# Performance work log

Hardware: AMD Instinct MI355X
Metric: run time of the kernel (lower is better)

Reference implementation:

```python
import jax, jax.numpy as jnp
import numpy as np

K = 20          # number of NAG iterations (init kwarg k)
MU = 0.05       # strong-convexity constant mu (init kwarg, fixed so no eigendecomp)
B, N = 4096, 128


def setup_inputs() -> dict:
    key = jax.random.key(0)
    k1, k2 = jax.random.split(key)
    w = jax.random.normal(k1, (B, N, N), dtype=jnp.float32)
    b = jax.random.normal(k2, (B, N), dtype=jnp.float32)
    s = jnp.asarray(1e-3, dtype=jnp.float32)  # learned step-size Parameter
    return {"w": w, "b": b, "s": s}


def reference(w, b, s):
    # NAG.forward with mu fixed, x_init=y_init=None (zeros), return_all=False.
    mu = jnp.asarray(MU, dtype=s.dtype)
    sqms = jnp.sqrt(mu * s)
    alpha = (1.0 - sqms) / (1.0 + sqms)  # scalar momentum coefficient

    x0 = jnp.zeros_like(b)
    y0 = jnp.zeros_like(b)

    def step(carry, _):
        x, y = carry
        # GD.gradient_decent(s, y, w, b): x_next = y - s * (w @ y - b)
        grad = jnp.einsum('bij,bj->bi', w, y) - b
        x_next = y - s * grad
        y_new = (1.0 + alpha) * x_next - alpha * x
        return (x_next, y_new), None

    (x, y), _ = jax.lax.scan(step, (x0, y0), None, length=K)
    return (x, y)
```

## Files before the change

### kernel.cpp

```cpp
#include <hip/hip_runtime.h>

#define K_ITERS 20
#define MU_CONST 0.05f
#define BN 128
#define YSTRIDE 24

typedef float v4f __attribute__((ext_vector_type(4)));
typedef __attribute__((address_space(1))) const v4f gc4;
typedef __attribute__((address_space(1))) v4f g4;

template <int CTRL>
__device__ __forceinline__ float dpp_add(float v) {
    int x = __builtin_amdgcn_update_dpp(0, __float_as_int(v), CTRL, 0xF, 0xF, true);
    return v + __int_as_float(x);
}
__device__ __forceinline__ float reduce8(float v) {
    v = dpp_add<0xB1>(v);
    v = dpp_add<0x4E>(v);
    v = dpp_add<0x141>(v);
    return v;
}

__global__ __launch_bounds__(256, 4) void nag_kernel(
    const float* __restrict__ w,
    const float* __restrict__ bvec,
    const float* __restrict__ s_ptr,
    float* __restrict__ out,
    int B)
{
    __shared__ __align__(16) float y_lds[2][8 * YSTRIDE];

    const int t  = threadIdx.x;
    const int wv = t >> 6;
    const int q  = (t >> 3) & 7;
    const int g  = t & 7;
    const int row0   = wv * 32 + q * 4;
    const int wslice = (row0 >> 4) * YSTRIDE + (q & 3) * 4;
    const int rbase  = g * YSTRIDE;

    const int batch = blockIdx.x;

    v4f w4[4][4];
    const gc4* wp = (const gc4*)(w + (size_t)batch * (BN * BN)
                                   + (size_t)row0 * BN + g * 16);
#pragma unroll
    for (int rho = 0; rho < 4; ++rho)
#pragma unroll
        for (int k = 0; k < 4; ++k)
            w4[rho][k] = wp[rho * 32 + k];

    const v4f br4 = *(const gc4*)(bvec + (size_t)batch * BN + row0);
    const float br_[4] = {br4.x, br4.y, br4.z, br4.w};

    const float s     = *s_ptr;
    const float sqms  = sqrtf(MU_CONST * s);
    const float alpha = (1.0f - sqms) / (1.0f + sqms);
    const float ap1   = 1.0f + alpha;

    float xs[4], ys[4];
#pragma unroll
    for (int rho = 0; rho < 4; ++rho) {
        xs[rho] = s * br_[rho];
        ys[rho] = ap1 * xs[rho];
    }
    if (g == 0)
        *reinterpret_cast<v4f*>(&y_lds[0][wslice]) =
            (v4f){ys[0], ys[1], ys[2], ys[3]};
    __syncthreads();

#pragma unroll 2
    for (int it = 1; it < K_ITERS; ++it) {
        const float* yb = &y_lds[(it + 1) & 1][rbase];
        v4f yv[4];
#pragma unroll
        for (int k = 0; k < 4; ++k)
            yv[k] = *reinterpret_cast<const v4f*>(yb + k * 4);

#pragma unroll
        for (int rho = 0; rho < 4; ++rho) {
            float p = w4[rho][0].x * yv[0].x;
            p = fmaf(w4[rho][0].y, yv[0].y, p);
            p = fmaf(w4[rho][0].z, yv[0].z, p);
            p = fmaf(w4[rho][0].w, yv[0].w, p);
            p = fmaf(w4[rho][1].x, yv[1].x, p);
            p = fmaf(w4[rho][1].y, yv[1].y, p);
            p = fmaf(w4[rho][1].z, yv[1].z, p);
            p = fmaf(w4[rho][1].w, yv[1].w, p);
            p = fmaf(w4[rho][2].x, yv[2].x, p);
            p = fmaf(w4[rho][2].y, yv[2].y, p);
            p = fmaf(w4[rho][2].z, yv[2].z, p);
            p = fmaf(w4[rho][2].w, yv[2].w, p);
            p = fmaf(w4[rho][3].x, yv[3].x, p);
            p = fmaf(w4[rho][3].y, yv[3].y, p);
            p = fmaf(w4[rho][3].z, yv[3].z, p);
            p = fmaf(w4[rho][3].w, yv[3].w, p);
            const float d  = reduce8(p);
            const float xn = fmaf(-s, d - br_[rho], ys[rho]);
            ys[rho] = fmaf(ap1, xn, -(alpha * xs[rho]));
            xs[rho] = xn;
        }

        if (it != K_ITERS - 1 && g == 0)
            *reinterpret_cast<v4f*>(&y_lds[it & 1][wslice]) =
                (v4f){ys[0], ys[1], ys[2], ys[3]};
        __syncthreads();
    }

    const size_t ob = (size_t)batch * BN + row0;
    if (g == 0)
        *(g4*)(out + ob) = (v4f){xs[0], xs[1], xs[2], xs[3]};
    else if (g == 1)
        *(g4*)(out + (size_t)B * BN + ob) = (v4f){ys[0], ys[1], ys[2], ys[3]};
}

extern "C" void kernel_launch(void* const* d_in, const int* in_sizes, int n_in,
                              void* d_out, int out_size, void* d_ws, size_t ws_size,
                              hipStream_t stream) {
    const float* w = (const float*)d_in[0];
    const float* b = (const float*)d_in[1];
    const float* s = (const float*)d_in[2];
    float* out = (float*)d_out;
    const int B = in_sizes[1] / BN;
    nag_kernel<<<dim3(B), dim3(256), 0, stream>>>(w, b, s, out, B);
}
```

Measured before the change: 60.67 us.

## Stage W loads through LDS with double-buffered direct global-to-LDS copies

Each wave now pulls its 32-row slice of W into a per-wave, double-buffered LDS staging area using global_load_lds, four sub-chunks at a time. Explicit vmcnt and lgkmcnt waits keep two chunks in flight while threads copy their rows from LDS into registers. The aim is fully coalesced, contiguous global reads and overlap of load latency with the register fill. In exchange it adds 32KB of LDS per block, which may limit occupancy, plus an extra LDS round trip on a kernel that is largely bandwidth bound.

```diff
diff --git a/kernel.cpp b/kernel.cpp
--- a/kernel.cpp
+++ b/kernel.cpp
@@ -4,10 +4,13 @@
 #define MU_CONST 0.05f
 #define BN 128
 #define YSTRIDE 24
+#define NSUBS 4
 
 typedef float v4f __attribute__((ext_vector_type(4)));
 typedef __attribute__((address_space(1))) const v4f gc4;
 typedef __attribute__((address_space(1))) v4f g4;
+typedef const __attribute__((address_space(1))) void* gas_ptr;
+typedef __attribute__((address_space(3))) void* las_ptr;
 
 template <int CTRL>
 __device__ __forceinline__ float dpp_add(float v) {
@@ -28,28 +31,66 @@
     float* __restrict__ out,
     int B)
 {
+    __shared__ __align__(16) float stage_lds[4][2][1024];
     __shared__ __align__(16) float y_lds[2][8 * YSTRIDE];
 
-    const int t  = threadIdx.x;
-    const int wv = t >> 6;
-    const int q  = (t >> 3) & 7;
-    const int g  = t & 7;
+    const int t    = threadIdx.x;
+    const int lane = t & 63;
+    const int wv   = t >> 6;
+    const int q    = (t >> 3) & 7;
+    const int g    = t & 7;
     const int row0   = wv * 32 + q * 4;
     const int wslice = (row0 >> 4) * YSTRIDE + (q & 3) * 4;
     const int rbase  = g * YSTRIDE;
 
     const int batch = blockIdx.x;
 
+    const v4f br4 = *(const gc4*)(bvec + (size_t)batch * BN + row0);
+
+    const float* wchunk = w + (size_t)batch * (BN * BN) + (size_t)(wv * 32) * BN;
+
+    auto stage = [&](int s) {
+        const int p = s & 1;
+#pragma unroll
+        for (int j = 0; j < 4; ++j)
+            __builtin_amdgcn_global_load_lds(
+                (gas_ptr)(wchunk + s * 1024 + j * 256 + lane * 4),
+                (las_ptr)(&stage_lds[wv][p][j * 256]), 16, 0, 0);
+    };
+
     v4f w4[4][4];
-    const gc4* wp = (const gc4*)(w + (size_t)batch * (BN * BN)
-                                   + (size_t)row0 * BN + g * 16);
+
+    stage(0);
+    stage(1);
 #pragma unroll
-    for (int rho = 0; rho < 4; ++rho)
+    for (int s = 0; s < NSUBS; ++s) {
+        __builtin_amdgcn_sched_barrier(0);
+        if (s < NSUBS - 1) asm volatile("s_waitcnt vmcnt(4)");
+        else               asm volatile("s_waitcnt vmcnt(0)");
+        __builtin_amdgcn_sched_barrier(0);
+
+        if ((q >> 1) == s) {
+            const float* sp = &stage_lds[wv][s & 1][0];
+            const int r_in = (q & 1) * 4;
 #pragma unroll
-        for (int k = 0; k < 4; ++k)
-            w4[rho][k] = wp[rho * 32 + k];
+            for (int rr = 0; rr < 4; ++rr)
+#pragma unroll
+                for (int k = 0; k < 4; ++k)
+                    w4[rr][k] = *reinterpret_cast<const v4f*>(
+                        sp + (r_in + rr) * BN + g * 16 + k * 4);
+        }
 
-    const v4f br4 = *(const gc4*)(bvec + (size_t)batch * BN + row0);
+        if (s + 2 < NSUBS) {
+            __builtin_amdgcn_sched_barrier(0);
+            asm volatile("s_waitcnt lgkmcnt(0)");
+            __builtin_amdgcn_sched_barrier(0);
+            stage(s + 2);
+        }
+    }
+    __builtin_amdgcn_sched_barrier(0);
+    asm volatile("s_waitcnt lgkmcnt(0)");
+    __builtin_amdgcn_sched_barrier(0);
+
     const float br_[4] = {br4.x, br4.y, br4.z, br4.w};
 
     const float s     = *s_ptr;
```

Measured after the change: 66.00 us. +8.8%, slower.
